# Kernel optimization log

Hardware: AMD Instinct MI355X
Metric: run time of the kernel (lower is better)

Reference implementation:

```python
import jax, jax.numpy as jnp
import numpy as np
import math

L, D, H, PK, N = 3, 512, 8, 8, 3072
DK = D // H


def _layernorm(x, s, b):
    m = jnp.mean(x, axis=-1, keepdims=True)
    v = jnp.mean((x - m) ** 2, axis=-1, keepdims=True)
    return (x - m) / jnp.sqrt(v + 1e-6) * s + b


def setup_inputs() -> dict:
    key = jax.random.key(0)
    ks = jax.random.split(key, 12)
    p = lambda k, shape: jax.random.normal(k, shape, jnp.float32) * (1.0 / math.sqrt(shape[-1]))
    x = jax.random.normal(ks[0], (N, D), jnp.float32)
    adm = jax.random.randint(ks[1], (N, N), 0, PK, jnp.int32)
    return {
        "x": x,
        "adm": adm,
        "ln_att_s": jnp.ones((L, D), jnp.float32),
        "ln_att_b": jnp.zeros((L, D), jnp.float32),
        "Wq": p(ks[2], (L, D, D)),
        "Wk": p(ks[3], (L, D, D)),
        "Wv": p(ks[4], (L, D, D)),
        "rel_k": p(ks[5], (L, PK, DK)),
        "Wg": p(ks[6], (L, D, D)) * 0.0,  # gating weight init to 0 in original
        "bg": jnp.ones((L, D), jnp.float32),  # gating bias init to 1
        "Wo": p(ks[7], (L, D, D)),
        "bo": jnp.zeros((L, D), jnp.float32),
        "ln_ff_s": jnp.ones((L, D), jnp.float32),
        "ln_ff_b": jnp.zeros((L, D), jnp.float32),
        "W1": p(ks[8], (L, D, 2 * D)),
        "b1": jnp.zeros((L, 2 * D), jnp.float32),
        "W2": p(ks[9], (L, 2 * D, D)),
        "b2": jnp.zeros((L, D), jnp.float32),
    }


def reference(x, adm, ln_att_s, ln_att_b, Wq, Wk, Wv, rel_k, Wg, bg, Wo, bo,
              ln_ff_s, ln_ff_b, W1, b1, W2, b2):
    att_scores = []
    idx = jnp.broadcast_to(adm[None], (H, N, N))  # one_hot(gpm) @ r  ==  gather r along PK
    for n in range(L):
        xn = _layernorm(x, ln_att_s[n], ln_att_b[n])  # same layer_norm applied to x_q and x_k
        q = (xn @ Wq[n]).reshape(N, H, DK).transpose(1, 0, 2)  # [H,N,DK]
        k = (xn @ Wk[n]).reshape(N, H, DK).transpose(1, 0, 2)
        v = (xn @ Wv[n]).reshape(N, H, DK).transpose(1, 0, 2)
        attn1 = jnp.einsum('hid,hjd->hij', q, k)  # [H,N,N]
        rq = jnp.einsum('hid,pd->hip', q, rel_k[n])  # [H,N,PK]
        attn2 = jnp.take_along_axis(rq, idx, axis=2)  # [H,N,N]
        attn = jax.nn.softmax((attn1 + attn2) / math.sqrt(DK), axis=-1)
        out = jnp.einsum('hij,hjd->hid', attn, v).transpose(1, 0, 2).reshape(N, D)
        gate = jax.nn.sigmoid(xn @ Wg[n] + bg[n])
        m = (out * gate) @ Wo[n] + bo[n]
        # FFN with pre-layernorm, residual: x = x + pff(x + m)
        y = x + m
        yn = _layernorm(y, ln_ff_s[n], ln_ff_b[n])
        ff = jax.nn.gelu(yn @ W1[n] + b1[n], approximate=True) @ W2[n] + b2[n]
        x = x + ff
        att_scores.append(attn)
    return (x, jnp.stack(att_scores))
```

## Files before the change

kernel.cpp:

```cpp
#include <hip/hip_runtime.h>
#include <math.h>

#define NT 3072
#define DIM 512
#define NH 8
#define DKH 64
#define PKN 8
#define D2 1024
#define NL 3
#define QS 2048

typedef float4 f4;
typedef unsigned short ushort_t;
typedef unsigned char uchar_t;
typedef __attribute__((ext_vector_type(8))) short s8x;
typedef __attribute__((ext_vector_type(4))) float fx4;

#define MFMA(a, b, c) __builtin_amdgcn_mfma_f32_16x16x32_bf16(a, b, c, 0, 0, 0)
#define EX2(x) __builtin_amdgcn_exp2f(x)

__device__ __forceinline__ float b2f(ushort_t u) {
  union { unsigned int x; float f; } c;
  c.x = (unsigned int)u << 16;
  return c.f;
}
__device__ __forceinline__ ushort_t f2b(float f) {
  union { float f; unsigned int x; } c;
  c.f = f;
  unsigned int r = (c.x + 0x7FFFu + ((c.x >> 16) & 1u)) >> 16;
  return (ushort_t)r;
}
__device__ __forceinline__ float wred_sum(float v) {
#pragma unroll
  for (int off = 32; off > 0; off >>= 1) v += __shfl_xor(v, off);
  return v;
}
__device__ __forceinline__ void gload16(const ushort_t* g, ushort_t* l) {
  __builtin_amdgcn_global_load_lds(
      (const __attribute__((address_space(1))) unsigned int*)(const void*)g,
      (__attribute__((address_space(3))) unsigned int*)(void*)l, 16, 0, 0);
}

__global__ __launch_bounds__(256) void ln_bf16_kernel(
    const float* __restrict__ x, const float* __restrict__ s,
    const float* __restrict__ b, ushort_t* __restrict__ out) {
  int row = blockIdx.x;
  const float* xr = x + (size_t)row * DIM;
  int t = threadIdx.x;
  float v0 = xr[t], v1 = xr[t + 256];
  float sum = wred_sum(v0 + v1);
  float sq = wred_sum(v0 * v0 + v1 * v1);
  __shared__ float ss[4], s2[4];
  if ((t & 63) == 0) { ss[t >> 6] = sum; s2[t >> 6] = sq; }
  __syncthreads();
  float tot = ss[0] + ss[1] + ss[2] + ss[3];
  float tot2 = s2[0] + s2[1] + s2[2] + s2[3];
  float mean = tot * (1.0f / DIM);
  float var = tot2 * (1.0f / DIM) - mean * mean;
  float inv = rsqrtf(var + 1e-6f);
  ushort_t* orow = out + (size_t)row * DIM;
  orow[t] = f2b((v0 - mean) * inv * s[t] + b[t]);
  orow[t + 256] = f2b((v1 - mean) * inv * s[t + 256] + b[t + 256]);
}

__device__ __forceinline__ void tconv_body(const float* __restrict__ W,
                                           ushort_t* __restrict__ Wt, int K,
                                           int Nc, int tx, int ty) {
  __shared__ float Ls[64][65];
  int t = threadIdx.x;
  int n0 = tx * 64, k0 = ty * 64;
  int rr = t >> 4, cc = (t & 15) * 4;
#pragma unroll
  for (int p = 0; p < 4; ++p) {
    f4 v = *(const f4*)&W[(size_t)(k0 + rr + p * 16) * Nc + n0 + cc];
    Ls[rr + p * 16][cc + 0] = v.x;
    Ls[rr + p * 16][cc + 1] = v.y;
    Ls[rr + p * 16][cc + 2] = v.z;
    Ls[rr + p * 16][cc + 3] = v.w;
  }
  __syncthreads();
  int nr = t >> 2, kc = (t & 3) * 16;
  ushort_t tmp[16];
#pragma unroll
  for (int e = 0; e < 16; ++e) tmp[e] = f2b(Ls[kc + e][nr]);
  ushort_t* dst = &Wt[(size_t)(n0 + nr) * K + k0 + kc];
  *(uint4*)dst = *(uint4*)&tmp[0];
  *(uint4*)(dst + 8) = *(uint4*)&tmp[8];
}

__global__ __launch_bounds__(256) void wprep_kernel(
    const float* __restrict__ Wq, const float* __restrict__ Wk,
    const float* __restrict__ Wv, const float* __restrict__ Wg,
    const float* __restrict__ Wo, const float* __restrict__ W1,
    const float* __restrict__ W2, ushort_t* __restrict__ Wt) {
  int n = blockIdx.y;
  size_t wo5 = (size_t)n * 262144;
  ushort_t* Wtl = Wt + (size_t)n * 2359296;
  int bid = blockIdx.x;
  if (bid < 320) {
    int job = bid >> 6, tile = bid & 63;
    const float* src = job == 0 ? Wq + wo5 : job == 1 ? Wk + wo5
                       : job == 2 ? Wv + wo5 : job == 3 ? Wg + wo5 : Wo + wo5;
    tconv_body(src, Wtl + (size_t)job * 262144, 512, 512, tile & 7, tile >> 3);
  } else if (bid < 448) {
    int tile = bid - 320;
    tconv_body(W1 + (size_t)n * 524288, Wtl + 1310720, 512, 1024, tile & 15,
               tile >> 4);
  } else {
    int tile = bid - 448;
    tconv_body(W2 + (size_t)n * 524288, Wtl + 1835008, 1024, 512, tile & 7,
               tile >> 3);
  }
}

__global__ __launch_bounds__(256) void adm8_kernel(const int* __restrict__ adm,
                                                   uchar_t* __restrict__ out) {
  size_t i = ((size_t)blockIdx.x * 256 + threadIdx.x) * 4;
  int4 v = *(const int4*)&adm[i];
  unsigned int b = (unsigned)(v.x & 255) | ((unsigned)(v.y & 255) << 8) |
                   ((unsigned)(v.z & 255) << 16) | ((unsigned)(v.w & 255) << 24);
  *(unsigned int*)&out[i] = b;
}

template <int ACT, bool OBF>
__global__ __launch_bounds__(256) void gemm64(
    const ushort_t* __restrict__ A, const ushort_t* __restrict__ Bt,
    const float* __restrict__ bias, const float* __restrict__ res,
    void* __restrict__ Cp, int K, int ldc, float scale,
    ushort_t* __restrict__ vt_out) {
  __shared__ __align__(16) ushort_t As[2][4096];
  __shared__ __align__(16) ushort_t Bs[2][4096];
  int t = threadIdx.x;
  int i0 = blockIdx.y * 64, j0 = blockIdx.x * 64;
  int w = t >> 6, l = t & 63;
  int wm = w >> 1, wn = w & 1;
  int lr = l >> 4, lc = l & 15;
  int sr = t >> 3;
  int sc8 = ((t & 7) ^ (sr & 7)) * 8;
  const ushort_t* aS = A + (size_t)(i0 + sr) * K + sc8;
  const ushort_t* bS = Bt + (size_t)(j0 + sr) * K + sc8;
  int sA0 = (wm * 32 + lc) * 64 + ((lr ^ (lc & 7)) * 8);
  int sA1 = (wm * 32 + 16 + lc) * 64 + ((lr ^ (lc & 7)) * 8);
  int sB0 = (wn * 32 + lc) * 64 + ((lr ^ (lc & 7)) * 8);
  int sB1 = (wn * 32 + 16 + lc) * 64 + ((lr ^ (lc & 7)) * 8);

  fx4 acc[2][2] = {};

#define G64_STAGE(buf, k0)                                                   \
  {                                                                          \
    gload16(aS + (k0), &As[buf][t * 8]);                                     \
    gload16(aS + (k0) + (size_t)32 * K, &As[buf][2048 + t * 8]);             \
    gload16(bS + (k0), &Bs[buf][t * 8]);                                     \
    gload16(bS + (k0) + (size_t)32 * K, &Bs[buf][2048 + t * 8]);             \
  }

  G64_STAGE(0, 0);
  __syncthreads();
  int cur = 0;
  for (int k0 = 0; k0 < K; k0 += 64) {
    if (k0 + 64 < K) G64_STAGE(cur ^ 1, k0 + 64);
    const ushort_t* Ac = As[cur];
    const ushort_t* Bc = Bs[cur];
#pragma unroll
    for (int ks = 0; ks < 2; ++ks) {
      s8x a0 = *(const s8x*)&Ac[sA0 ^ (ks << 5)];
      s8x a1 = *(const s8x*)&Ac[sA1 ^ (ks << 5)];
      s8x b0 = *(const s8x*)&Bc[sB0 ^ (ks << 5)];
      s8x b1 = *(const s8x*)&Bc[sB1 ^ (ks << 5)];
      acc[0][0] = MFMA(a0, b0, acc[0][0]);
      acc[0][1] = MFMA(a0, b1, acc[0][1]);
      acc[1][0] = MFMA(a1, b0, acc[1][0]);
      acc[1][1] = MFMA(a1, b1, acc[1][1]);
    }
    __syncthreads();
    cur ^= 1;
  }
#undef G64_STAGE

  bool isV = (ACT == 3) && (blockIdx.x >= 16) && (blockIdx.x < 24);
  ushort_t* TrS = &As[0][0];

#pragma unroll
  for (int ms = 0; ms < 2; ++ms) {
#pragma unroll
    for (int ns = 0; ns < 2; ++ns) {
      ushort_t vtmp[4];
#pragma unroll
      for (int r = 0; r < 4; ++r) {
        int i = i0 + wm * 32 + ms * 16 + lr * 4 + r;
        int j = j0 + wn * 32 + ns * 16 + lc;
        float o = acc[ms][ns][r] * scale;
        if (ACT == 3) {
          if (blockIdx.x < 8) o *= 0.18033688011112042f;
          if (blockIdx.x >= 24) {
            o += bias[j & 511];
            o = 1.0f / (1.0f + __expf(-o));
          }
        } else {
          if (bias) o += bias[j];
          if (ACT == 1) {
            o = 1.0f / (1.0f + __expf(-o));
          } else if (ACT == 2) {
            float xx = o;
            float c2 = 1.5957691216057308f * (xx + 0.044715f * xx * xx * xx);
            o = xx / (1.0f + __expf(-c2));
          }
          if (res) o += res[(size_t)i * ldc + j];
        }
        if (OBF) {
          ushort_t ob = f2b(o);
          ((ushort_t*)Cp)[(size_t)i * ldc + j] = ob;
          if (isV) vtmp[r] = ob;
        } else {
          ((float*)Cp)[(size_t)i * ldc + j] = o;
        }
      }
      if (isV) {
        int jl = wn * 32 + ns * 16 + lc;
        int ib = wm * 32 + ms * 16 + lr * 4;
        *(uint2*)&TrS[jl * 64 + (ib ^ ((jl & 7) << 3))] = *(uint2*)vtmp;
      }
    }
  }
  if (isV) {
    __syncthreads();
    int d = t >> 2, c = (t & 3) * 16;
    int sw8 = (d & 7) << 3;
    uint4 A_ = *(const uint4*)&TrS[d * 64 + (c ^ sw8)];
    uint4 B_ = *(const uint4*)&TrS[d * 64 + ((c + 8) ^ sw8)];
    ushort_t* dst =
        vt_out + (size_t)((blockIdx.x - 16) * 64 + d) * NT + i0 + c;
    *(uint4*)dst = A_;
    *(uint4*)(dst + 8) = B_;
  }
}

__device__ __forceinline__ float rq_sel(const unsigned int* rqt,
                                        unsigned int idx) {
  unsigned int d01 = (idx & 2) ? rqt[1] : rqt[0];
  unsigned int d23 = (idx & 2) ? rqt[3] : rqt[2];
  unsigned int dd = (idx & 4) ? d23 : d01;
  unsigned int r = (idx & 1) ? (dd & 0xffff0000u) : (dd << 16);
  return __uint_as_float(r);
}

__global__ __launch_bounds__(256) void attn_ml_kernel(
    const ushort_t* __restrict__ xqkvg, const float* __restrict__ relk,
    const uchar_t* __restrict__ adm8, float* __restrict__ lofsb) {
  int f = blockIdx.y * (NT / 32) + blockIdx.x;
  int h = f & 7;
  int i0 = (f >> 3) * 32;
  int t = threadIdx.x, w = t >> 6, l = t & 63;
  int lr = l >> 4, lc = l & 15;
  int ig = w & 1, jh = w >> 1;
  int i_loc = ig * 16 + lc;
  int i = i0 + i_loc;

  __shared__ __align__(16) ushort_t Kd[2][2][4096];
  __shared__ float MLs[2][2][16];

  int stgo = ig * 2048;
  int srow = ig * 32 + (l >> 3);
  int kp8 = ((l & 7) ^ ((l >> 3) & 7)) * 8;
  const ushort_t* kSrc0 =
      xqkvg + 512 + (size_t)(jh * 64 + srow) * QS + h * 64 + kp8;
  const uchar_t* admp0 = adm8 + (size_t)i * NT + jh * 64 + lr * 4;

#define STAGE_K1(buf, tt)                                                    \
  {                                                                          \
    const ushort_t* ks_ = kSrc0 + (size_t)(tt) * 128 * QS;                   \
    gload16(ks_, Kd[buf][jh] + stgo);                                        \
    gload16(ks_ + (size_t)8 * QS, Kd[buf][jh] + stgo + 512);                 \
    gload16(ks_ + (size_t)16 * QS, Kd[buf][jh] + stgo + 1024);               \
    gload16(ks_ + (size_t)24 * QS, Kd[buf][jh] + stgo + 1536);               \
  }

  STAGE_K1(0, 0);

  const ushort_t* qp = xqkvg + (size_t)i * QS + h * 64 + lr * 8;
  s8x qf0 = *(const s8x*)qp;
  s8x qf1 = *(const s8x*)(qp + 32);

  unsigned int rqt[4];
  {
    const ushort_t* q0 = (const ushort_t*)&qf0;
    const ushort_t* q1 = (const ushort_t*)&qf1;
    float sp[8];
#pragma unroll
    for (int p = 0; p < 8; ++p) {
      const float* rp = relk + p * 64 + lr * 8;
      float s = 0.f;
#pragma unroll
      for (int e = 0; e < 8; ++e) s = fmaf(b2f(q0[e]), rp[e], s);
#pragma unroll
      for (int e = 0; e < 8; ++e) s = fmaf(b2f(q1[e]), rp[32 + e], s);
      s += __shfl_xor(s, 16);
      s += __shfl_xor(s, 32);
      sp[p] = s;
    }
#pragma unroll
    for (int j = 0; j < 4; ++j)
      rqt[j] = (unsigned int)f2b(sp[2 * j]) |
               ((unsigned int)f2b(sp[2 * j + 1]) << 16);
  }

  int sw = (lc & 7);
  int a_b0 = lc * 64 + ((lr ^ sw) << 3);
  int a_b1 = lc * 64 + (((4 + lr) ^ sw) << 3);

  float l_run = 0.f;
  __syncthreads();

  int cur = 0;
  for (int tt = 0; tt < 24; ++tt) {
    if (tt < 23) STAGE_K1(cur ^ 1, tt + 1);
    const ushort_t* KS = Kd[cur][jh];
    const uchar_t* admp = admp0 + tt * 128;
    fx4 sacc[4] = {};
#pragma unroll
    for (int ja = 0; ja < 4; ++ja) {
      s8x a0 = *(const s8x*)(KS + a_b0 + ja * 1024);
      s8x a1 = *(const s8x*)(KS + a_b1 + ja * 1024);
      sacc[ja] = MFMA(a0, qf0, sacc[ja]);
      sacc[ja] = MFMA(a1, qf1, sacc[ja]);
    }
    float sum = 0.f;
#pragma unroll
    for (int ja = 0; ja < 4; ++ja) {
      unsigned int aw = *(const unsigned int*)(admp + ja * 16);
#pragma unroll
      for (int r = 0; r < 4; ++r)
        sum += EX2(sacc[ja][r] + rq_sel(rqt, (aw >> (8 * r)) & 7u));
    }
    l_run += sum;
    __syncthreads();
    cur ^= 1;
  }
#undef STAGE_K1

  l_run += __shfl_xor(l_run, 16);
  l_run += __shfl_xor(l_run, 32);
  if (l < 16) MLs[jh][ig][lc] = l_run;
  __syncthreads();
  if (jh == 0 && l < 16)
    lofsb[(size_t)h * NT + i] = __log2f(l_run + MLs[1][ig][lc]);
}

__global__ __launch_bounds__(256) void attn_pv_kernel(
    const ushort_t* __restrict__ xqkvg, const ushort_t* __restrict__ vbT,
    const float* __restrict__ relk, const uchar_t* __restrict__ adm8,
    const float* __restrict__ lofsb, float* __restrict__ att,
    ushort_t* __restrict__ av) {
  int f = blockIdx.y * (NT / 32) + blockIdx.x;
  int h = f & 7;
  int i0 = (f >> 3) * 32;
  int t = threadIdx.x, w = t >> 6, l = t & 63;
  int lr = l >> 4, lc = l & 15;
  int ig = w & 1, jh = w >> 1;
  int i_loc = ig * 16 + lc;
  int i = i0 + i_loc;

  __shared__ __align__(16) ushort_t Kd[2][2][4096];
  __shared__ __align__(16) ushort_t Vd[2][2][4096];
  __shared__ __align__(16) ushort_t Ps[2][2048];

  int stgo = ig * 2048;
  int srow = ig * 32 + (l >> 3);
  int kp8 = ((l & 7) ^ ((l >> 3) & 7)) * 8;
  const ushort_t* kSrc0 =
      xqkvg + 512 + (size_t)(jh * 64 + srow) * QS + h * 64 + kp8;
  const ushort_t* vSrc0 = vbT + (size_t)(h * 64 + srow) * NT + jh * 64 + kp8;
  const uchar_t* admp0 = adm8 + (size_t)i * NT + jh * 64 + lr * 4;

#define STAGE_K2(buf, tt)                                                    \
  {                                                                          \
    const ushort_t* ks_ = kSrc0 + (size_t)(tt) * 128 * QS;                   \
    gload16(ks_, Kd[buf][jh] + stgo);                                        \
    gload16(ks_ + (size_t)8 * QS, Kd[buf][jh] + stgo + 512);                 \
    gload16(ks_ + (size_t)16 * QS, Kd[buf][jh] + stgo + 1024);               \
    gload16(ks_ + (size_t)24 * QS, Kd[buf][jh] + stgo + 1536);               \
  }
#define STAGE_V2(buf, tt)                                                    \
  {                                                                          \
    const ushort_t* vs_ = vSrc0 + (tt) * 128;                                \
    gload16(vs_, Vd[buf][jh] + stgo);                                        \
    gload16(vs_ + (size_t)8 * NT, Vd[buf][jh] + stgo + 512);                 \
    gload16(vs_ + (size_t)16 * NT, Vd[buf][jh] + stgo + 1024);               \
    gload16(vs_ + (size_t)24 * NT, Vd[buf][jh] + stgo + 1536);               \
  }

  STAGE_K2(0, 0);
  STAGE_V2(0, 0);

  const ushort_t* qp = xqkvg + (size_t)i * QS + h * 64 + lr * 8;
  s8x qf0 = *(const s8x*)qp;
  s8x qf1 = *(const s8x*)(qp + 32);
  float lofs = lofsb[(size_t)h * NT + i];

  unsigned int rqt[4];
  {
    const ushort_t* q0 = (const ushort_t*)&qf0;
    const ushort_t* q1 = (const ushort_t*)&qf1;
    float sp[8];
#pragma unroll
    for (int p = 0; p < 8; ++p) {
      const float* rp = relk + p * 64 + lr * 8;
      float s = 0.f;
#pragma unroll
      for (int e = 0; e < 8; ++e) s = fmaf(b2f(q0[e]), rp[e], s);
#pragma unroll
      for (int e = 0; e < 8; ++e) s = fmaf(b2f(q1[e]), rp[32 + e], s);
      s += __shfl_xor(s, 16);
      s += __shfl_xor(s, 32);
      sp[p] = s;
    }
#pragma unroll
    for (int j = 0; j < 4; ++j)
      rqt[j] = (unsigned int)f2b(sp[2 * j]) |
               ((unsigned int)f2b(sp[2 * j + 1]) << 16);
  }

  int sw = (lc & 7);
  int a_b0 = lc * 64 + ((lr ^ sw) << 3);
  int a_b1 = lc * 64 + (((4 + lr) ^ sw) << 3);
  int pb0 = i_loc * 64 + ((lr ^ sw) << 3);
  int pb1 = i_loc * 64 + (((4 + lr) ^ sw) << 3);
  int swz8 = sw << 3;

  fx4 oacc[4] = {};
  float* attb = att + ((size_t)h * NT + i0) * NT;
  ushort_t* PS = Ps[jh];
  int jh64 = jh * 64;
  __syncthreads();

  int cur = 0;
  for (int tt = 0; tt < 24; ++tt) {
    if (tt < 23) {
      STAGE_K2(cur ^ 1, tt + 1);
      STAGE_V2(cur ^ 1, tt + 1);
    }
    const ushort_t* KS = Kd[cur][jh];
    const ushort_t* VS = Vd[cur][jh];
    const uchar_t* admp = admp0 + tt * 128;
    fx4 sacc[4] = {};
#pragma unroll
    for (int ja = 0; ja < 4; ++ja) {
      s8x a0 = *(const s8x*)(KS + a_b0 + ja * 1024);
      s8x a1 = *(const s8x*)(KS + a_b1 + ja * 1024);
      sacc[ja] = MFMA(a0, qf0, sacc[ja]);
      sacc[ja] = MFMA(a1, qf1, sacc[ja]);
    }
#pragma unroll
    for (int ja = 0; ja < 4; ++ja) {
      unsigned int aw = *(const unsigned int*)(admp + ja * 16);
      float p0 = EX2(sacc[ja][0] + rq_sel(rqt, aw & 7u) - lofs);
      float p1 = EX2(sacc[ja][1] + rq_sel(rqt, (aw >> 8) & 7u) - lofs);
      float p2 = EX2(sacc[ja][2] + rq_sel(rqt, (aw >> 16) & 7u) - lofs);
      float p3 = EX2(sacc[ja][3] + rq_sel(rqt, (aw >> 24) & 7u) - lofs);
      unsigned int w01 = (unsigned int)f2b(p0) | ((unsigned int)f2b(p1) << 16);
      unsigned int w23 = (unsigned int)f2b(p2) | ((unsigned int)f2b(p3) << 16);
      int cb = ja * 16 + lr * 4;
      *(unsigned int*)&PS[i_loc * 64 + (cb ^ swz8)] = w01;
      *(unsigned int*)&PS[i_loc * 64 + ((cb + 2) ^ swz8)] = w23;
    }
    {
      int uu = ig * 64 + l;
      int row = uu >> 2, cs = (uu & 3) * 16;
      int rsw = (row & 7) << 3;
      uint4 A_ = *(const uint4*)&PS[row * 64 + (cs ^ rsw)];
      uint4 B_ = *(const uint4*)&PS[row * 64 + ((cs + 8) ^ rsw)];
      const ushort_t* ap = (const ushort_t*)&A_;
      const ushort_t* bp = (const ushort_t*)&B_;
      float* op = attb + (size_t)row * NT + tt * 128 + jh64 + cs;
      f4 o0 = {b2f(ap[0]), b2f(ap[1]), b2f(ap[2]), b2f(ap[3])};
      f4 o1 = {b2f(ap[4]), b2f(ap[5]), b2f(ap[6]), b2f(ap[7])};
      f4 o2 = {b2f(bp[0]), b2f(bp[1]), b2f(bp[2]), b2f(bp[3])};
      f4 o3 = {b2f(bp[4]), b2f(bp[5]), b2f(bp[6]), b2f(bp[7])};
      *(f4*)(op + 0) = o0;
      *(f4*)(op + 4) = o1;
      *(f4*)(op + 8) = o2;
      *(f4*)(op + 12) = o3;
    }
#pragma unroll
    for (int ks = 0; ks < 2; ++ks) {
      s8x pf = *(const s8x*)(PS + (ks == 0 ? pb0 : pb1));
#pragma unroll
      for (int nd = 0; nd < 4; ++nd) {
        s8x vf = *(const s8x*)(VS + (ks == 0 ? a_b0 : a_b1) + nd * 1024);
        oacc[nd] = MFMA(vf, pf, oacc[nd]);
      }
    }
    __syncthreads();
    cur ^= 1;
  }
#undef STAGE_K2
#undef STAGE_V2

  ushort_t* PsF = &Ps[0][0];
  int swzO = (i_loc & 7) << 3;
  if (jh == 1) {
#pragma unroll
    for (int nd = 0; nd < 4; ++nd) {
      int d0 = nd * 16 + lr * 4;
      unsigned int lo = (unsigned int)f2b(oacc[nd][0]) |
                        ((unsigned int)f2b(oacc[nd][1]) << 16);
      unsigned int hi = (unsigned int)f2b(oacc[nd][2]) |
                        ((unsigned int)f2b(oacc[nd][3]) << 16);
      uint2 pk = {lo, hi};
      *(uint2*)&PsF[i_loc * 64 + (d0 ^ swzO)] = pk;
    }
  }
  __syncthreads();
  if (jh == 0) {
    const ushort_t* gp = xqkvg + (size_t)i * QS + 1536 + h * 64;
#pragma unroll
    for (int nd = 0; nd < 4; ++nd) {
      int d0 = nd * 16 + lr * 4;
      uint2 pk = *(const uint2*)&PsF[i_loc * 64 + (d0 ^ swzO)];
      const ushort_t* pp = (const ushort_t*)&pk;
      uint2 gk = *(const uint2*)(gp + d0);
      const ushort_t* gg = (const ushort_t*)&gk;
      ushort_t ot[4];
#pragma unroll
      for (int r = 0; r < 4; ++r)
        ot[r] = f2b((oacc[nd][r] + b2f(pp[r])) * b2f(gg[r]));
      *(uint2*)&av[(size_t)i * DIM + h * 64 + d0] = *(uint2*)ot;
    }
  }
}

extern "C" void kernel_launch(void* const* d_in, const int* in_sizes, int n_in,
                              void* d_out, int out_size, void* d_ws,
                              size_t ws_size, hipStream_t stream) {
  const float* x_in = (const float*)d_in[0];
  const int* adm = (const int*)d_in[1];
  const float* ln_att_s = (const float*)d_in[2];
  const float* ln_att_b = (const float*)d_in[3];
  const float* Wq = (const float*)d_in[4];
  const float* Wk = (const float*)d_in[5];
  const float* Wv = (const float*)d_in[6];
  const float* rel_k = (const float*)d_in[7];
  const float* Wg = (const float*)d_in[8];
  const float* bg = (const float*)d_in[9];
  const float* Wo = (const float*)d_in[10];
  const float* bo = (const float*)d_in[11];
  const float* ln_ff_s = (const float*)d_in[12];
  const float* ln_ff_b = (const float*)d_in[13];
  const float* W1 = (const float*)d_in[14];
  const float* b1 = (const float*)d_in[15];
  const float* W2 = (const float*)d_in[16];
  const float* b2 = (const float*)d_in[17];
  float* out = (float*)d_out;

  const size_t ND = (size_t)NT * DIM;
  char* ws = (char*)d_ws;
  float* x_cur = (float*)ws;
  float* y = (float*)(ws + 6291456);
  ushort_t* xqkvg = (ushort_t*)(ws + 12582912);
  ushort_t* avb = (ushort_t*)(ws + 25165824);
  ushort_t* xnb = (ushort_t*)(ws + 28311552);
  ushort_t* vbT = (ushort_t*)(ws + 31457280);
  uchar_t* adm8 = (uchar_t*)(ws + 34603008);
  float* lofsb = (float*)(ws + 44040192);
  ushort_t* Wt = (ushort_t*)(ws + 44138496);
  ushort_t* h1b = xqkvg;

  adm8_kernel<<<(NT * NT) / 1024, 256, 0, stream>>>(adm, adm8);
  wprep_kernel<<<dim3(576, 3), 256, 0, stream>>>(Wq, Wk, Wv, Wg, Wo, W1, W2,
                                                 Wt);

  dim3 gQKVG(32, NT / 64);
  dim3 gA(8, NT / 64);
  dim3 gF1(16, NT / 64);
  dim3 gATT(NT / 32, NH);

  for (int n = 0; n < NL; ++n) {
    float* att = out + ND + (size_t)n * NH * NT * NT;
    const float* xprev = (n == 0) ? x_in : x_cur;
    float* xout = (n == NL - 1) ? out : x_cur;
    ushort_t* Wtl = Wt + (size_t)n * 2359296;

    ln_bf16_kernel<<<NT, 256, 0, stream>>>(xprev, ln_att_s + n * DIM,
                                           ln_att_b + n * DIM, xnb);
    gemm64<3, true><<<gQKVG, 256, 0, stream>>>(xnb, Wtl, bg + n * DIM, nullptr,
                                               xqkvg, DIM, QS, 1.0f, vbT);
    attn_ml_kernel<<<gATT, 256, 0, stream>>>(xqkvg, rel_k + n * PKN * DKH,
                                             adm8, lofsb);
    attn_pv_kernel<<<gATT, 256, 0, stream>>>(
        xqkvg, vbT, rel_k + n * PKN * DKH, adm8, lofsb, att, avb);
    gemm64<0, false><<<gA, 256, 0, stream>>>(avb, Wtl + 1048576, bo + n * DIM,
                                             xprev, y, DIM, DIM, 1.0f, nullptr);
    ln_bf16_kernel<<<NT, 256, 0, stream>>>(y, ln_ff_s + n * DIM,
                                           ln_ff_b + n * DIM, xnb);
    gemm64<2, true><<<gF1, 256, 0, stream>>>(xnb, Wtl + 1310720, b1 + n * D2,
                                             nullptr, h1b, DIM, D2, 1.0f,
                                             nullptr);
    gemm64<0, false><<<gA, 256, 0, stream>>>(h1b, Wtl + 1835008, b2 + n * DIM,
                                             xprev, xout, D2, DIM, 1.0f,
                                             nullptr);
  }
}
```

Baseline: 0.9998 ms.

## Read K fragments directly from global memory instead of staging through LDS

Both attention kernels stop double-buffering K tiles into shared memory and load the MFMA A-fragments for K straight from global memory, relying on L1/L2. In the row-sum kernel this also removes all block barriers and re-splits the key range so each half-block walks a contiguous 1536-key chunk. The intent is to cut LDS traffic, shared-memory footprint and synchronisation, which may raise occupancy. The trade-off is uncoalesced 16-byte global loads per lane, with latency no longer hidden by async prefetch.

Measured after the change: 1.157 ms. +15.7%, slower.

```diff
diff --git a/kernel.cpp b/kernel.cpp
--- a/kernel.cpp
+++ b/kernel.cpp
@@ -253,29 +253,9 @@
   int t = threadIdx.x, w = t >> 6, l = t & 63;
   int lr = l >> 4, lc = l & 15;
   int ig = w & 1, jh = w >> 1;
-  int i_loc = ig * 16 + lc;
-  int i = i0 + i_loc;
-
-  __shared__ __align__(16) ushort_t Kd[2][2][4096];
+  int i = i0 + ig * 16 + lc;
+
   __shared__ float MLs[2][2][16];
-
-  int stgo = ig * 2048;
-  int srow = ig * 32 + (l >> 3);
-  int kp8 = ((l & 7) ^ ((l >> 3) & 7)) * 8;
-  const ushort_t* kSrc0 =
-      xqkvg + 512 + (size_t)(jh * 64 + srow) * QS + h * 64 + kp8;
-  const uchar_t* admp0 = adm8 + (size_t)i * NT + jh * 64 + lr * 4;
-
-#define STAGE_K1(buf, tt)                                                    \
-  {                                                                          \
-    const ushort_t* ks_ = kSrc0 + (size_t)(tt) * 128 * QS;                   \
-    gload16(ks_, Kd[buf][jh] + stgo);                                        \
-    gload16(ks_ + (size_t)8 * QS, Kd[buf][jh] + stgo + 512);                 \
-    gload16(ks_ + (size_t)16 * QS, Kd[buf][jh] + stgo + 1024);               \
-    gload16(ks_ + (size_t)24 * QS, Kd[buf][jh] + stgo + 1536);               \
-  }
-
-  STAGE_K1(0, 0);
 
   const ushort_t* qp = xqkvg + (size_t)i * QS + h * 64 + lr * 8;
   s8x qf0 = *(const s8x*)qp;
@@ -304,26 +284,23 @@
                ((unsigned int)f2b(sp[2 * j + 1]) << 16);
   }
 
-  int sw = (lc & 7);
-  int a_b0 = lc * 64 + ((lr ^ sw) << 3);
-  int a_b1 = lc * 64 + (((4 + lr) ^ sw) << 3);
+  const ushort_t* kbase =
+      xqkvg + 512 + (size_t)(jh * 1536 + lc) * QS + h * 64 + lr * 8;
+  const uchar_t* admp0 = adm8 + (size_t)i * NT + jh * 1536 + lr * 4;
 
   float l_run = 0.f;
-  __syncthreads();
-
-  int cur = 0;
   for (int tt = 0; tt < 24; ++tt) {
-    if (tt < 23) STAGE_K1(cur ^ 1, tt + 1);
-    const ushort_t* KS = Kd[cur][jh];
-    const uchar_t* admp = admp0 + tt * 128;
+    const ushort_t* kp = kbase + (size_t)(tt * 64) * QS;
     fx4 sacc[4] = {};
 #pragma unroll
     for (int ja = 0; ja < 4; ++ja) {
-      s8x a0 = *(const s8x*)(KS + a_b0 + ja * 1024);
-      s8x a1 = *(const s8x*)(KS + a_b1 + ja * 1024);
+      const ushort_t* kj = kp + (size_t)(ja * 16) * QS;
+      s8x a0 = *(const s8x*)kj;
+      s8x a1 = *(const s8x*)(kj + 32);
       sacc[ja] = MFMA(a0, qf0, sacc[ja]);
       sacc[ja] = MFMA(a1, qf1, sacc[ja]);
     }
+    const uchar_t* admp = admp0 + tt * 64;
     float sum = 0.f;
 #pragma unroll
     for (int ja = 0; ja < 4; ++ja) {
@@ -333,10 +310,7 @@
         sum += EX2(sacc[ja][r] + rq_sel(rqt, (aw >> (8 * r)) & 7u));
     }
     l_run += sum;
-    __syncthreads();
-    cur ^= 1;
-  }
-#undef STAGE_K1
+  }
 
   l_run += __shfl_xor(l_run, 16);
   l_run += __shfl_xor(l_run, 32);
@@ -360,26 +334,15 @@
   int i_loc = ig * 16 + lc;
   int i = i0 + i_loc;
 
-  __shared__ __align__(16) ushort_t Kd[2][2][4096];
   __shared__ __align__(16) ushort_t Vd[2][2][4096];
   __shared__ __align__(16) ushort_t Ps[2][2048];
 
   int stgo = ig * 2048;
   int srow = ig * 32 + (l >> 3);
   int kp8 = ((l & 7) ^ ((l >> 3) & 7)) * 8;
-  const ushort_t* kSrc0 =
-      xqkvg + 512 + (size_t)(jh * 64 + srow) * QS + h * 64 + kp8;
   const ushort_t* vSrc0 = vbT + (size_t)(h * 64 + srow) * NT + jh * 64 + kp8;
   const uchar_t* admp0 = adm8 + (size_t)i * NT + jh * 64 + lr * 4;
 
-#define STAGE_K2(buf, tt)                                                    \
-  {                                                                          \
-    const ushort_t* ks_ = kSrc0 + (size_t)(tt) * 128 * QS;                   \
-    gload16(ks_, Kd[buf][jh] + stgo);                                        \
-    gload16(ks_ + (size_t)8 * QS, Kd[buf][jh] + stgo + 512);                 \
-    gload16(ks_ + (size_t)16 * QS, Kd[buf][jh] + stgo + 1024);               \
-    gload16(ks_ + (size_t)24 * QS, Kd[buf][jh] + stgo + 1536);               \
-  }
 #define STAGE_V2(buf, tt)                                                    \
   {                                                                          \
     const ushort_t* vs_ = vSrc0 + (tt) * 128;                                \
@@ -389,7 +352,6 @@
     gload16(vs_ + (size_t)24 * NT, Vd[buf][jh] + stgo + 1536);               \
   }
 
-  STAGE_K2(0, 0);
   STAGE_V2(0, 0);
 
   const ushort_t* qp = xqkvg + (size_t)i * QS + h * 64 + lr * 8;
@@ -427,6 +389,9 @@
   int pb1 = i_loc * 64 + (((4 + lr) ^ sw) << 3);
   int swz8 = sw << 3;
 
+  const ushort_t* kbase =
+      xqkvg + 512 + (size_t)(jh * 64 + lc) * QS + h * 64 + lr * 8;
+
   fx4 oacc[4] = {};
   float* attb = att + ((size_t)h * NT + i0) * NT;
   ushort_t* PS = Ps[jh];
@@ -435,18 +400,16 @@
 
   int cur = 0;
   for (int tt = 0; tt < 24; ++tt) {
-    if (tt < 23) {
-      STAGE_K2(cur ^ 1, tt + 1);
-      STAGE_V2(cur ^ 1, tt + 1);
-    }
-    const ushort_t* KS = Kd[cur][jh];
+    if (tt < 23) STAGE_V2(cur ^ 1, tt + 1);
     const ushort_t* VS = Vd[cur][jh];
+    const ushort_t* kp = kbase + (size_t)(tt * 128) * QS;
     const uchar_t* admp = admp0 + tt * 128;
     fx4 sacc[4] = {};
 #pragma unroll
     for (int ja = 0; ja < 4; ++ja) {
-      s8x a0 = *(const s8x*)(KS + a_b0 + ja * 1024);
-      s8x a1 = *(const s8x*)(KS + a_b1 + ja * 1024);
+      const ushort_t* kj = kp + (size_t)(ja * 16) * QS;
+      s8x a0 = *(const s8x*)kj;
+      s8x a1 = *(const s8x*)(kj + 32);
       sacc[ja] = MFMA(a0, qf0, sacc[ja]);
       sacc[ja] = MFMA(a1, qf1, sacc[ja]);
     }
@@ -493,7 +456,6 @@
     __syncthreads();
     cur ^= 1;
   }
-#undef STAGE_K2
 #undef STAGE_V2
 
   ushort_t* PsF = &Ps[0][0];
```
